# Kernel optimization log

Measured on AMD Instinct MI355X. Metric: run time of the kernel, lower is better.

## Reference

```python
import jax, jax.numpy as jnp
from jax import lax
import numpy as np

# ---- static APPM geometry (MMAL-Net config: input 448, stride 32 -> 14x14 fm) ----
STRIDE = 32
FM = 14
RATIOS = [[4, 4], [3, 5], [5, 3],
          [6, 6], [5, 7], [7, 5],
          [8, 8], [6, 10], [10, 6], [7, 9], [9, 7], [7, 10], [10, 7]]
N_LIST = [3, 2, 1]          # proposals per ratio-group -> proposalN = 6
IOU_THRESHS = [0.25, 0.25, 0.25]
GROUP_RATIO_SPLITS = [3, 6, 13]  # ratios 0:3, 3:6, 6:13


def _window_num(r):
    return (FM - r[0] + 1) * (FM - r[1] + 1)


def _build_coords():
    # indices2coordinates: window (i,j) of ratio (rh,rw) -> pixel box, inclusive ends
    coords = []
    for rh, rw in RATIOS:
        rows, cols = FM - rh + 1, FM - rw + 1
        ii, jj = np.meshgrid(np.arange(rows), np.arange(cols), indexing='ij')
        x0 = ii.reshape(-1) * STRIDE
        y0 = jj.reshape(-1) * STRIDE
        x1 = x0 + rh * STRIDE - 1
        y1 = y0 + rw * STRIDE - 1
        coords.append(np.stack([x0, y0, x1, y1], 1))
    return np.concatenate(coords, 0).astype(np.float32)

COORDS = jnp.asarray(_build_coords())  # [917, 4]
WINDOW_NUMS = [_window_num(r) for r in RATIOS]
_g1 = sum(WINDOW_NUMS[:3]); _g2 = sum(WINDOW_NUMS[3:6]); _g3 = sum(WINDOW_NUMS[6:])
GROUPS = [(0, _g1), (_g1, _g1 + _g2), (_g1 + _g2, _g1 + _g2 + _g3)]  # (0,361),(361,602),(602,917)


def _argmax_mask(logits):
    # mask = 0.7 everywhere, 1.0 at per-row argmax
    B, C = logits.shape
    one_hot = jax.nn.one_hot(jnp.argmax(logits, axis=1), C, dtype=logits.dtype)
    return 0.7 + 0.3 * one_hot


def _nms_group(scores, coords, n_pick, thresh):
    # greedy descending-score NMS; scores [W], coords [W,4]
    x0, y0, x1, y1 = coords[:, 0], coords[:, 1], coords[:, 2], coords[:, 3]
    areas = (x1 - x0 + 1.0) * (y1 - y0 + 1.0)

    def step(carry, _):
        valid, last = carry
        masked = jnp.where(valid, scores, -jnp.inf)
        idx = jnp.argmax(masked).astype(jnp.int32)
        idx = jnp.where(valid.any(), idx, last)  # pad by repeating last pick
        ix0, iy0, ix1, iy1 = coords[idx]
        lx = jnp.minimum(x1, ix1) - jnp.maximum(x0, ix0) + 1.0
        ly = jnp.minimum(y1, iy1) - jnp.maximum(y0, iy0) + 1.0
        inter = jnp.where((lx < 0) | (ly < 0), 0.0, lx * ly)
        iou = inter / (areas + areas[idx] - inter)
        valid = valid & (iou <= thresh)  # also suppresses idx itself (iou == 1)
        return (valid, idx), idx

    init = (jnp.ones(scores.shape[0], dtype=bool), jnp.int32(0))
    (_, _), picks = lax.scan(step, init, None, length=n_pick)
    return picks  # [n_pick] int32


def _appm(local_fm):
    # avgpool over each ratio then sum over channels == channel-sum then 2D mean pool
    B = local_fm.shape[0]
    fm_sum = jnp.sum(local_fm, axis=1)  # [B,14,14]
    per_ratio = []
    for rh, rw in RATIOS:
        pooled = lax.reduce_window(fm_sum, jnp.float32(0.0), lax.add,
                                   (1, rh, rw), (1, 1, 1), 'VALID') / (rh * rw)
        per_ratio.append(pooled.reshape(B, -1))
    all_scores = jnp.concatenate(per_ratio, axis=1)  # [B, 917]

    picks = []
    for (s, e), n_pick, thr in zip(GROUPS, N_LIST, IOU_THRESHS):
        g = jax.vmap(lambda sc: _nms_group(sc, COORDS[s:e], n_pick, thr))(all_scores[:, s:e])
        picks.append(g + s)
    proposalN_indices = jnp.concatenate(picks, axis=1)  # [B, 6]
    proposalN_windows_scores = jnp.take_along_axis(all_scores, proposalN_indices, axis=1)
    return proposalN_indices, proposalN_windows_scores, all_scores


def setup_inputs() -> dict:
    key = jax.random.key(0)
    ks = jax.random.split(key, 6)
    B, C, NC, BIT = 256, 512, 200, 48
    return {
        'local_fm': jax.random.normal(ks[0], (B, C, 14, 14), jnp.float32),
        'local_embeddings': jax.random.normal(ks[1], (B, C), jnp.float32),
        'W_cls': jax.random.normal(ks[2], (NC, C), jnp.float32) * 0.02,
        'b_cls': jax.random.normal(ks[3], (NC,), jnp.float32) * 0.02,
        'W_hash': jax.random.normal(ks[4], (BIT, NC), jnp.float32) * 0.02,
        'b_hash': jax.random.normal(ks[5], (BIT,), jnp.float32) * 0.02,
    }


def reference(local_fm, local_embeddings, W_cls, b_cls, W_hash, b_hash):
    # classification head + per-row argmax masking + hash head (Tanh)
    local_logits = local_embeddings @ W_cls.T + b_cls          # [B, num_classes]
    masked = local_logits * _argmax_mask(local_logits)
    local_hash_code = jnp.tanh(masked @ W_hash.T + b_hash)     # [B, bit]
    # APPM region proposal on detached feature map
    proposalN_indices, proposalN_windows_scores, window_scores = _appm(
        lax.stop_gradient(local_fm))
    return (local_hash_code, local_logits, proposalN_indices,
            proposalN_windows_scores, window_scores)
```

## Files before the change

### kernel.cpp

```cpp
#include <hip/hip_runtime.h>
#include <math.h>

#define NW 917

__constant__ int c_off[13]  = {0,121,241,361,442,522,602,651,696,741,789,837,877};
__constant__ int c_rh[13]   = {4,3,5,6,5,7,8,6,10,7,9,7,10};
__constant__ int c_rw[13]   = {4,5,3,6,7,5,8,10,6,9,7,10,7};
__constant__ int c_cols[13] = {11,10,12,9,8,10,7,5,9,6,8,5,8};

__device__ inline void decode_w(int w, int& r, int& i, int& j){
    int rr = 0;
    #pragma unroll
    for (int k = 1; k < 13; ++k) if (w >= c_off[k]) rr = k;
    int loc = w - c_off[rr];
    int cols = c_cols[rr];
    r = rr; i = loc / cols; j = loc - i * cols;
}

__device__ inline unsigned long long nms_key(float v, int w){
    unsigned u = __float_as_uint(v);
    u = (u & 0x80000000u) ? ~u : (u | 0x80000000u);
    return ((unsigned long long)u << 32) | (unsigned)(0xFFFFFFFFu - (unsigned)w);
}

__device__ inline unsigned long long shfl_xor_u64(unsigned long long x, int m){
    unsigned lo = (unsigned)x, hi = (unsigned)(x >> 32);
    lo = __shfl_xor(lo, m);
    hi = __shfl_xor(hi, m);
    return ((unsigned long long)hi << 32) | lo;
}

__global__ __launch_bounds__(1024) void mono_kernel(const float* __restrict__ fm,
                                                    const float* __restrict__ E,
                                                    const float* __restrict__ Wc,
                                                    const float* __restrict__ bc,
                                                    const float* __restrict__ Wh,
                                                    const float* __restrict__ bh,
                                                    float* __restrict__ out_hash,
                                                    float* __restrict__ out_logits,
                                                    float* __restrict__ out_idx,
                                                    float* __restrict__ out_psc,
                                                    float* __restrict__ out_scores){
    int b = blockIdx.x, t = threadIdx.x;
    int lane = t & 63, wv = t >> 6;

    __shared__ float4 red[16][49];
    __shared__ float fmS[196];
    __shared__ float R[14][15];
    __shared__ float I[15][15];
    __shared__ float s[NW];
    __shared__ unsigned long long wred[16];
    __shared__ float emb[512];
    __shared__ float lg[200];
    __shared__ float mk[200];

    const float4* base = (const float4*)(fm + (size_t)b * 512 * 196);
    if (lane < 49){
        float4 acc = {0.f,0.f,0.f,0.f};
        int c0 = wv * 32;
        #pragma unroll 8
        for (int k = 0; k < 32; ++k){
            float4 v = base[(size_t)(c0 + k) * 49 + lane];
            acc.x += v.x; acc.y += v.y; acc.z += v.z; acc.w += v.w;
        }
        red[wv][lane] = acc;
    }
    if (t < 512) emb[t] = E[b * 512 + t];
    __syncthreads();
    if (t < 49){
        float4 a = red[0][t];
        #pragma unroll
        for (int k = 1; k < 16; ++k){
            float4 v = red[k][t];
            a.x += v.x; a.y += v.y; a.z += v.z; a.w += v.w;
        }
        ((float4*)fmS)[t] = a;
    }
    __syncthreads();

    if (t < 14){
        float run = 0.f;
        R[t][0] = 0.f;
        for (int j = 0; j < 14; ++j){ run += fmS[t * 14 + j]; R[t][j + 1] = run; }
    }
    __syncthreads();
    if (t < 15){
        float run = 0.f;
        I[0][t] = 0.f;
        for (int i = 0; i < 14; ++i){ run += R[i][t]; I[i + 1][t] = run; }
    }
    __syncthreads();

    if (t < NW){
        int r, i, j; decode_w(t, r, i, j);
        int rh = c_rh[r], rw = c_rw[r];
        float sum = I[i + rh][j + rw] - I[i][j + rw] - I[i + rh][j] + I[i][j];
        float sc = sum / (float)(rh * rw);
        s[t] = sc;
        out_scores[(size_t)b * NW + t] = sc;
    }
    __syncthreads();

    const int gs_[3] = {0, 361, 602};
    const int ge_[3] = {361, 602, NW};
    const int np_[3] = {3, 2, 1};
    int slot = 0;
    for (int g = 0; g < 3; ++g){
        int gs = gs_[g], m = ge_[g] - gs;
        bool has = t < m;
        int w0 = gs + t;
        float x0=0,y0=0,x1=0,y1=0,ar=1.f,sc=0.f;
        if (has){
            int r,i,j; decode_w(w0,r,i,j);
            x0 = i*32.f; y0 = j*32.f;
            x1 = x0 + c_rh[r]*32.f - 1.f; y1 = y0 + c_rw[r]*32.f - 1.f;
            ar = (float)(c_rh[r]*32 * c_rw[r]*32);
            sc = s[w0];
        }
        bool v = true;
        int last = 0;
        for (int p = 0; p < np_[g]; ++p){
            unsigned long long key = (has && v) ? nms_key(sc, w0) : 0ULL;
            #pragma unroll
            for (int off = 32; off > 0; off >>= 1){
                unsigned long long o = shfl_xor_u64(key, off);
                if (o > key) key = o;
            }
            if (lane == 0) wred[wv] = key;
            __syncthreads();
            unsigned long long best = wred[0];
            #pragma unroll
            for (int k = 1; k < 16; ++k) if (wred[k] > best) best = wred[k];
            int pick = (best == 0ULL) ? last
                                      : (int)(0xFFFFFFFFu - (unsigned)(best & 0xFFFFFFFFu));
            last = pick;
            int pr, pi, pj; decode_w(pick, pr, pi, pj);
            float px0 = pi*32.f, py0 = pj*32.f;
            float px1 = px0 + c_rh[pr]*32.f - 1.f, py1 = py0 + c_rw[pr]*32.f - 1.f;
            float pa  = (float)(c_rh[pr]*32 * c_rw[pr]*32);
            if (has && v){
                float lx = fminf(x1,px1) - fmaxf(x0,px0) + 1.f;
                float ly = fminf(y1,py1) - fmaxf(y0,py0) + 1.f;
                float inter = (lx < 0.f || ly < 0.f) ? 0.f : lx * ly;
                float iou = inter / (ar + pa - inter);
                v = (iou <= 0.25f);
            }
            if (t == 0){
                out_idx[b * 6 + slot] = (float)pick;
                out_psc[b * 6 + slot] = s[pick];
            }
            slot++;
            __syncthreads();
        }
    }

    float tot = 0.f;
    if (t < 400){
        int row = t >> 1, part = t & 1;
        const float4* w4 = (const float4*)(Wc + (size_t)row * 512) + part * 64;
        const float* e = emb + part * 256;
        float acc = (part == 0) ? bc[row] : 0.f;
        #pragma unroll 8
        for (int k = 0; k < 64; ++k){
            float4 w = w4[k];
            acc += e[4*k]*w.x + e[4*k+1]*w.y + e[4*k+2]*w.z + e[4*k+3]*w.w;
        }
        tot = acc + __shfl_xor(acc, 1);
        if (part == 0){
            lg[row] = tot;
            out_logits[(size_t)b * 200 + row] = tot;
        }
    }
    unsigned long long key = (t < 400 && !(t & 1)) ? nms_key(tot, t >> 1) : 0ULL;
    #pragma unroll
    for (int off = 32; off > 0; off >>= 1){
        unsigned long long o = shfl_xor_u64(key, off);
        if (o > key) key = o;
    }
    if (lane == 0) wred[wv] = key;
    __syncthreads();
    unsigned long long best = wred[0];
    #pragma unroll
    for (int k = 1; k < 16; ++k) if (wred[k] > best) best = wred[k];
    int amax = (int)(0xFFFFFFFFu - (unsigned)(best & 0xFFFFFFFFu));
    if (t < 200) mk[t] = lg[t] * (t == amax ? 1.0f : 0.7f);
    __syncthreads();
    if (t < 96){
        int row = t >> 1, part = t & 1;
        const float4* w4 = (const float4*)(Wh + (size_t)row * 200) + part * 25;
        const float* mm = mk + part * 100;
        float acc = (part == 0) ? bh[row] : 0.f;
        #pragma unroll
        for (int k = 0; k < 25; ++k){
            float4 w = w4[k];
            acc += mm[4*k]*w.x + mm[4*k+1]*w.y + mm[4*k+2]*w.z + mm[4*k+3]*w.w;
        }
        float tt = acc + __shfl_xor(acc, 1);
        if (part == 0) out_hash[b * 48 + row] = tanhf(tt);
    }
}

extern "C" void kernel_launch(void* const* d_in, const int* in_sizes, int n_in,
                              void* d_out, int out_size, void* d_ws, size_t ws_size,
                              hipStream_t stream) {
    const float* fm = (const float*)d_in[0];
    const float* E  = (const float*)d_in[1];
    const float* Wc = (const float*)d_in[2];
    const float* bc = (const float*)d_in[3];
    const float* Wh = (const float*)d_in[4];
    const float* bh = (const float*)d_in[5];
    float* out        = (float*)d_out;
    float* out_hash   = out;
    float* out_logits = out + 12288;
    float* out_idx    = out + 63488;
    float* out_psc    = out + 65024;
    float* out_scores = out + 66560;

    hipLaunchKernelGGL(mono_kernel, dim3(256), dim3(1024), 0, stream,
                       fm, E, Wc, bc, Wh, bh,
                       out_hash, out_logits, out_idx, out_psc, out_scores);
}
```

Measured before the change: 180.0 us.

## Run NMS in one wavefront concurrently with classifier GEMV on other waves

The NMS now runs entirely in wavefront 0, with each lane holding 15 windows in registers. This removes the per-pick block-wide __syncthreads and shared-memory reductions. The remaining 15 wavefronts compute the classifier logits at the same time, using 16 lanes per row with coalesced float4 loads. The feature-map channel reduction is rebalanced across 980 threads so loads are contiguous, the logit argmax moves to per-wave shuffles, and the hash GEMV uses 16 lanes per row. The trade-off is higher register pressure in wave 0 and NMS work serialized in a single wave.

```diff
diff --git a/kernel.cpp b/kernel.cpp
--- a/kernel.cpp
+++ b/kernel.cpp
@@ -44,33 +44,37 @@
     int b = blockIdx.x, t = threadIdx.x;
     int lane = t & 63, wv = t >> 6;
 
-    __shared__ float4 red[16][49];
+    __shared__ float4 red[20][49];
     __shared__ float fmS[196];
     __shared__ float R[14][15];
     __shared__ float I[15][15];
     __shared__ float s[NW];
-    __shared__ unsigned long long wred[16];
     __shared__ float emb[512];
     __shared__ float lg[200];
     __shared__ float mk[200];
 
     const float4* base = (const float4*)(fm + (size_t)b * 512 * 196);
-    if (lane < 49){
+    if (t < 980){
+        int cg = t / 49;
+        const float4* p4 = base + t;
         float4 acc = {0.f,0.f,0.f,0.f};
-        int c0 = wv * 32;
-        #pragma unroll 8
-        for (int k = 0; k < 32; ++k){
-            float4 v = base[(size_t)(c0 + k) * 49 + lane];
+        #pragma unroll 5
+        for (int k = 0; k < 25; ++k){
+            float4 v = p4[980 * k];
             acc.x += v.x; acc.y += v.y; acc.z += v.z; acc.w += v.w;
         }
-        red[wv][lane] = acc;
+        if (cg < 12){
+            float4 v = p4[980 * 25];
+            acc.x += v.x; acc.y += v.y; acc.z += v.z; acc.w += v.w;
+        }
+        red[cg][t - cg * 49] = acc;
     }
     if (t < 512) emb[t] = E[b * 512 + t];
     __syncthreads();
     if (t < 49){
         float4 a = red[0][t];
         #pragma unroll
-        for (int k = 1; k < 16; ++k){
+        for (int k = 1; k < 20; ++k){
             float4 v = red[k][t];
             a.x += v.x; a.y += v.y; a.z += v.z; a.w += v.w;
         }
@@ -101,102 +105,141 @@
     }
     __syncthreads();
 
-    const int gs_[3] = {0, 361, 602};
-    const int ge_[3] = {361, 602, NW};
-    const int np_[3] = {3, 2, 1};
-    int slot = 0;
-    for (int g = 0; g < 3; ++g){
-        int gs = gs_[g], m = ge_[g] - gs;
-        bool has = t < m;
-        int w0 = gs + t;
-        float x0=0,y0=0,x1=0,y1=0,ar=1.f,sc=0.f;
-        if (has){
-            int r,i,j; decode_w(w0,r,i,j);
-            x0 = i*32.f; y0 = j*32.f;
-            x1 = x0 + c_rh[r]*32.f - 1.f; y1 = y0 + c_rw[r]*32.f - 1.f;
-            ar = (float)(c_rh[r]*32 * c_rw[r]*32);
-            sc = s[w0];
-        }
-        bool v = true;
-        int last = 0;
-        for (int p = 0; p < np_[g]; ++p){
-            unsigned long long key = (has && v) ? nms_key(sc, w0) : 0ULL;
-            #pragma unroll
-            for (int off = 32; off > 0; off >>= 1){
-                unsigned long long o = shfl_xor_u64(key, off);
-                if (o > key) key = o;
+    if (wv == 0){
+        float sc_[15]; unsigned pk_[15]; int gr_[15];
+        #pragma unroll
+        for (int m = 0; m < 15; ++m){
+            int w = lane + (m << 6);
+            bool ok = w < NW;
+            int r = 0, i = 0, j = 0;
+            if (ok) decode_w(w, r, i, j);
+            sc_[m] = ok ? s[w] : 0.f;
+            pk_[m] = (unsigned)(i | (j << 4) | (c_rh[r] << 8) | (c_rw[r] << 12));
+            gr_[m] = ok ? ((w >= 602) ? 2 : (w >= 361) ? 1 : 0) : 3;
+        }
+        unsigned vmask = 0x7FFFu;
+        int slot = 0;
+        #pragma unroll
+        for (int g = 0; g < 3; ++g){
+            int npick = (g == 0) ? 3 : (g == 1) ? 2 : 1;
+            int last  = (g == 0) ? 0 : (g == 1) ? 361 : 602;
+            for (int p = 0; p < npick; ++p){
+                unsigned long long key = 0ULL;
+                #pragma unroll
+                for (int m = 0; m < 15; ++m){
+                    if (gr_[m] == g && ((vmask >> m) & 1u)){
+                        unsigned long long k2 = nms_key(sc_[m], lane + (m << 6));
+                        if (k2 > key) key = k2;
+                    }
+                }
+                #pragma unroll
+                for (int off = 32; off > 0; off >>= 1){
+                    unsigned long long o = shfl_xor_u64(key, off);
+                    if (o > key) key = o;
+                }
+                int pick = (key == 0ULL) ? last
+                                         : (int)(0xFFFFFFFFu - (unsigned)(key & 0xFFFFFFFFu));
+                last = pick;
+                int pr, pi, pj; decode_w(pick, pr, pi, pj);
+                float px0 = pi * 32.f, py0 = pj * 32.f;
+                float prh = (float)c_rh[pr], prw = (float)c_rw[pr];
+                float px1 = px0 + prh * 32.f - 1.f, py1 = py0 + prw * 32.f - 1.f;
+                float pa  = prh * prw * 1024.f;
+                #pragma unroll
+                for (int m = 0; m < 15; ++m){
+                    if (gr_[m] == g && ((vmask >> m) & 1u)){
+                        unsigned pk = pk_[m];
+                        float x0 = (float)(pk & 15u) * 32.f;
+                        float y0 = (float)((pk >> 4) & 15u) * 32.f;
+                        float rh = (float)((pk >> 8) & 15u);
+                        float rw = (float)(pk >> 12);
+                        float x1 = x0 + rh * 32.f - 1.f;
+                        float y1 = y0 + rw * 32.f - 1.f;
+                        float ar = rh * rw * 1024.f;
+                        float lx = fminf(x1, px1) - fmaxf(x0, px0) + 1.f;
+                        float ly = fminf(y1, py1) - fmaxf(y0, py0) + 1.f;
+                        float inter = (lx < 0.f || ly < 0.f) ? 0.f : lx * ly;
+                        float iou = inter / (ar + pa - inter);
+                        if (iou > 0.25f) vmask &= ~(1u << m);
+                    }
+                }
+                if (lane == 0){
+                    out_idx[b * 6 + slot] = (float)pick;
+                    out_psc[b * 6 + slot] = s[pick];
+                }
+                slot++;
             }
-            if (lane == 0) wred[wv] = key;
-            __syncthreads();
-            unsigned long long best = wred[0];
-            #pragma unroll
-            for (int k = 1; k < 16; ++k) if (wred[k] > best) best = wred[k];
-            int pick = (best == 0ULL) ? last
-                                      : (int)(0xFFFFFFFFu - (unsigned)(best & 0xFFFFFFFFu));
-            last = pick;
-            int pr, pi, pj; decode_w(pick, pr, pi, pj);
-            float px0 = pi*32.f, py0 = pj*32.f;
-            float px1 = px0 + c_rh[pr]*32.f - 1.f, py1 = py0 + c_rw[pr]*32.f - 1.f;
-            float pa  = (float)(c_rh[pr]*32 * c_rw[pr]*32);
-            if (has && v){
-                float lx = fminf(x1,px1) - fmaxf(x0,px0) + 1.f;
-                float ly = fminf(y1,py1) - fmaxf(y0,py0) + 1.f;
-                float inter = (lx < 0.f || ly < 0.f) ? 0.f : lx * ly;
-                float iou = inter / (ar + pa - inter);
-                v = (iou <= 0.25f);
+        }
+    } else {
+        int gw  = wv - 1;
+        int grp = lane >> 4;
+        int s16 = lane & 15;
+        const float4* emb4 = (const float4*)emb;
+        for (int p = 0; p < 4; ++p){
+            int row = p * 60 + gw * 4 + grp;
+            if (row < 200){
+                const float4* wrow = (const float4*)(Wc + (size_t)row * 512);
+                float acc = 0.f;
+                #pragma unroll
+                for (int k = 0; k < 8; ++k){
+                    float4 w = wrow[k * 16 + s16];
+                    float4 e = emb4[k * 16 + s16];
+                    acc += e.x * w.x + e.y * w.y + e.z * w.z + e.w * w.w;
+                }
+                acc += __shfl_xor(acc, 1);
+                acc += __shfl_xor(acc, 2);
+                acc += __shfl_xor(acc, 4);
+                acc += __shfl_xor(acc, 8);
+                if (s16 == 0){
+                    float v = acc + bc[row];
+                    lg[row] = v;
+                    out_logits[(size_t)b * 200 + row] = v;
+                }
             }
-            if (t == 0){
-                out_idx[b * 6 + slot] = (float)pick;
-                out_psc[b * 6 + slot] = s[pick];
-            }
-            slot++;
-            __syncthreads();
-        }
-    }
-
-    float tot = 0.f;
-    if (t < 400){
-        int row = t >> 1, part = t & 1;
-        const float4* w4 = (const float4*)(Wc + (size_t)row * 512) + part * 64;
-        const float* e = emb + part * 256;
-        float acc = (part == 0) ? bc[row] : 0.f;
-        #pragma unroll 8
-        for (int k = 0; k < 64; ++k){
-            float4 w = w4[k];
-            acc += e[4*k]*w.x + e[4*k+1]*w.y + e[4*k+2]*w.z + e[4*k+3]*w.w;
-        }
-        tot = acc + __shfl_xor(acc, 1);
-        if (part == 0){
-            lg[row] = tot;
-            out_logits[(size_t)b * 200 + row] = tot;
-        }
-    }
-    unsigned long long key = (t < 400 && !(t & 1)) ? nms_key(tot, t >> 1) : 0ULL;
-    #pragma unroll
-    for (int off = 32; off > 0; off >>= 1){
-        unsigned long long o = shfl_xor_u64(key, off);
-        if (o > key) key = o;
-    }
-    if (lane == 0) wred[wv] = key;
-    __syncthreads();
-    unsigned long long best = wred[0];
-    #pragma unroll
-    for (int k = 1; k < 16; ++k) if (wred[k] > best) best = wred[k];
-    int amax = (int)(0xFFFFFFFFu - (unsigned)(best & 0xFFFFFFFFu));
-    if (t < 200) mk[t] = lg[t] * (t == amax ? 1.0f : 0.7f);
-    __syncthreads();
-    if (t < 96){
-        int row = t >> 1, part = t & 1;
-        const float4* w4 = (const float4*)(Wh + (size_t)row * 200) + part * 25;
-        const float* mm = mk + part * 100;
-        float acc = (part == 0) ? bh[row] : 0.f;
-        #pragma unroll
-        for (int k = 0; k < 25; ++k){
-            float4 w = w4[k];
-            acc += mm[4*k]*w.x + mm[4*k+1]*w.y + mm[4*k+2]*w.z + mm[4*k+3]*w.w;
-        }
-        float tt = acc + __shfl_xor(acc, 1);
-        if (part == 0) out_hash[b * 48 + row] = tanhf(tt);
+        }
+    }
+    __syncthreads();
+
+    {
+        unsigned long long key = nms_key(lg[lane], lane);
+        unsigned long long k2  = nms_key(lg[lane + 64], lane + 64);
+        if (k2 > key) key = k2;
+        k2 = nms_key(lg[lane + 128], lane + 128);
+        if (k2 > key) key = k2;
+        if (lane + 192 < 200){
+            k2 = nms_key(lg[lane + 192], lane + 192);
+            if (k2 > key) key = k2;
+        }
+        #pragma unroll
+        for (int off = 32; off > 0; off >>= 1){
+            unsigned long long o = shfl_xor_u64(key, off);
+            if (o > key) key = o;
+        }
+        int amax = (int)(0xFFFFFFFFu - (unsigned)(key & 0xFFFFFFFFu));
+        if (t < 200) mk[t] = lg[t] * (t == amax ? 1.0f : 0.7f);
+    }
+    __syncthreads();
+
+    if (t < 768){
+        int row = t >> 4;
+        int s16 = t & 15;
+        const float4* wrow = (const float4*)(Wh + (size_t)row * 200);
+        const float4* mk4  = (const float4*)mk;
+        float4 w0 = wrow[s16],      m0 = mk4[s16];
+        float4 w1 = wrow[s16 + 16], m1 = mk4[s16 + 16];
+        float4 w2 = wrow[s16 + 32], m2 = mk4[s16 + 32];
+        float acc = w0.x*m0.x + w0.y*m0.y + w0.z*m0.z + w0.w*m0.w
+                  + w1.x*m1.x + w1.y*m1.y + w1.z*m1.z + w1.w*m1.w
+                  + w2.x*m2.x + w2.y*m2.y + w2.z*m2.z + w2.w*m2.w;
+        if (s16 < 2){
+            float4 w3 = wrow[s16 + 48], m3 = mk4[s16 + 48];
+            acc += w3.x*m3.x + w3.y*m3.y + w3.z*m3.z + w3.w*m3.w;
+        }
+        acc += __shfl_xor(acc, 1);
+        acc += __shfl_xor(acc, 2);
+        acc += __shfl_xor(acc, 4);
+        acc += __shfl_xor(acc, 8);
+        if (s16 == 0) out_hash[b * 48 + row] = tanhf(acc + bh[row]);
     }
 }
 
```

Result: faster. 170.0 us (-5.5%).
